# Kernel optimization log

Hardware: AMD Instinct MI355X
Metric: run time of the kernel (lower is better)

## Reference

```python
import jax, jax.numpy as jnp
import numpy as np

B = 32768
N_KPS = 14
DIM = N_KPS * 3   # 42
H1 = 1024
N_DOF = 7

# Fixed kinematic-chain constants (stand-in for the robot's link geometry,
# Franka-like link lengths; constants on device in the original).
LINK_LEN = jnp.array([0.333, 0.316, 0.384, 0.088, 0.107, 0.103, 0.100], dtype=jnp.float32)
OFF = jnp.array([0.05, 0.0, 0.0], dtype=jnp.float32)  # per-link auxiliary keypoint offset


def _rot_z(t):
    c, s = jnp.cos(t), jnp.sin(t)
    z, o = jnp.zeros_like(t), jnp.ones_like(t)
    return jnp.stack([jnp.stack([c, -s, z], -1),
                      jnp.stack([s, c, z], -1),
                      jnp.stack([z, z, o], -1)], -2)


def _rot_y(t):
    c, s = jnp.cos(t), jnp.sin(t)
    z, o = jnp.zeros_like(t), jnp.ones_like(t)
    return jnp.stack([jnp.stack([c, z, s], -1),
                      jnp.stack([z, o, z], -1),
                      jnp.stack([-s, z, c], -1)], -2)


def compute_3n_loss_42_rob(angles):
    """Forward kinematics: angles [B,7] -> keypoints [B,14,3].
    Alternating z/y revolute joints; 2 keypoints per link (origin + offset)."""
    Bn = angles.shape[0]
    R = jnp.broadcast_to(jnp.eye(3, dtype=angles.dtype), (Bn, 3, 3))
    p = jnp.zeros((Bn, 3), dtype=angles.dtype)
    pts = []
    for j in range(N_DOF):
        Rj = _rot_z(angles[:, j]) if j % 2 == 0 else _rot_y(angles[:, j])
        R = jnp.einsum('bij,bjk->bik', R, Rj)
        p = p + R @ jnp.array([0.0, 0.0, 1.0], dtype=angles.dtype) * LINK_LEN[j]
        pts.append(p)
        pts.append(p + R @ OFF)
    return jnp.stack(pts, axis=1)  # [B, 14, 3]


def compute_rede_rt(P, Q):
    """Batched Kabsch: rigid (R, t) minimizing ||R P + t - Q||. P,Q: [B,N,3]."""
    cp = P.mean(axis=1, keepdims=True)
    cq = Q.mean(axis=1, keepdims=True)
    H = jnp.einsum('bni,bnj->bij', P - cp, Q - cq)  # [B,3,3]
    U, S, Vt = jnp.linalg.svd(H)
    V = jnp.swapaxes(Vt, -1, -2)
    d = jnp.sign(jnp.linalg.det(jnp.einsum('bij,bkj->bik', V, U)))
    D = jnp.concatenate([jnp.ones((P.shape[0], 2), P.dtype), d[:, None]], axis=1)
    R = jnp.einsum('bij,bj,bkj->bik', V, D, U)  # V diag(1,1,d) U^T
    t = cq[:, 0] - jnp.einsum('bij,bj->bi', R, cp[:, 0])
    return R, t


def setup_inputs() -> dict:
    key = jax.random.key(0)
    k1, k2, k3, k4, k5 = jax.random.split(key, 5)
    return {
        'joints_3d_pred': jax.random.normal(k1, (B, N_KPS, 3), dtype=jnp.float32),
        'W1': jax.random.normal(k2, (DIM, H1), dtype=jnp.float32) * 0.05,
        'b1': jax.random.normal(k3, (H1,), dtype=jnp.float32) * 0.01,
        'W2': jax.random.normal(k4, (H1, N_DOF), dtype=jnp.float32) * 0.05,
        'b2': jax.random.normal(k5, (N_DOF,), dtype=jnp.float32) * 0.01,
    }


def reference(joints_3d_pred, W1, b1, W2, b2):
    # normalize to root keypoint
    norm = joints_3d_pred - joints_3d_pred[:, :1, :]          # [B,14,3]
    x = norm.reshape(norm.shape[0], -1)                        # [B,42]
    h = jax.nn.relu(x @ W1 + b1)                               # [B,1024]
    angles = h @ W2 + b2                                       # [B,7]
    all_dof_pred = angles[:, :, None]                          # [B,7,1]
    rob = compute_3n_loss_42_rob(angles)                       # [B,14,3]
    R, t = compute_rede_rt(rob, norm)
    t = t + joints_3d_pred[:, 0]                               # un-normalize translation
    top = jnp.concatenate([R, t[:, :, None]], axis=2)          # [B,3,4]
    bottom = jnp.broadcast_to(jnp.array([0.0, 0.0, 0.0, 1.0], dtype=R.dtype), (R.shape[0], 1, 4))
    pose = jnp.concatenate([top, bottom], axis=1)              # [B,4,4]
    return all_dof_pred, pose
```

## Files before the change

### kernel.cpp

```cpp
#include <hip/hip_runtime.h>
#include <math.h>

typedef __attribute__((ext_vector_type(8))) short short8;
typedef __attribute__((ext_vector_type(4))) float f32x4;
typedef __attribute__((ext_vector_type(2))) float f32x2;

constexpr int B_   = 32768;
constexpr int NKPS = 14;
constexpr int DIM  = 42;
constexpr int H1_  = 1024;
constexpr int NDOF = 7;

__device__ __forceinline__ unsigned short f2bf(float f) {
    unsigned u = __float_as_uint(f);
    u += 0x7FFFu + ((u >> 16) & 1u);
    return (unsigned short)(u >> 16);
}
__device__ __forceinline__ float bf2f(unsigned short h) {
    return __uint_as_float(((unsigned)h) << 16);
}

__global__ __launch_bounds__(256)
void prep_kernel(const float* __restrict__ W1, const float* __restrict__ b1,
                 const float* __restrict__ W2,
                 unsigned short* __restrict__ B1, float* __restrict__ W2p)
{
    const int T = blockIdx.x * 256 + threadIdx.x;
    if (T < 16384) {
        const int lane  = T & 63;
        const int ntile = (T >> 6) & 63;
        const int ks    = T >> 12;
        const int n     = ntile * 16 + (lane & 15);
        const int kbase = ks * 32 + ((lane >> 4) << 3);
        short8 s;
#pragma unroll
        for (int j = 0; j < 8; ++j) {
            const int k = kbase + j;
            unsigned short r;
            if (k < 42) {
                r = f2bf(W1[k * H1_ + n]);
            } else if (k < 84) {
                r = f2bf(W1[(k - 42) * H1_ + n]);
            } else if (k < 126) {
                const float x = W1[(k - 84) * H1_ + n];
                const unsigned short hi = f2bf(x);
                r = f2bf(x - bf2f(hi));
            } else if (k == 126) {
                r = f2bf(b1[n]);
            } else {
                const float x = b1[n];
                const unsigned short hi = f2bf(x);
                r = f2bf(x - bf2f(hi));
            }
            s[j] = (short)r;
        }
        *((short8*)(B1 + (long)T * 8)) = s;
    } else if (T < 16384 + 1024) {
        const int n = T - 16384;
#pragma unroll
        for (int d = 0; d < 7; ++d) W2p[n * 8 + d] = W2[n * 7 + d];
        W2p[n * 8 + 7] = 0.f;
    }
}

__global__ __launch_bounds__(512, 4)
void mlp_kernel(const float* __restrict__ joints,
                const unsigned short* __restrict__ B1,
                const float* __restrict__ W2p,
                const float* __restrict__ b2,
                float* __restrict__ outAng)
{
    __shared__ unsigned short Alds[32][136];
    __shared__ float sbuf[32][8];

    const int  tid = threadIdx.x;
    const long bm  = (long)blockIdx.x * 32;

    if (tid < 256) ((float*)sbuf)[tid] = 0.f;

    {
        const int r   = tid >> 4;
        const int c16 = tid & 15;
        const float* jr = joints + (bm + r) * DIM;
        short8 s;
#pragma unroll
        for (int j = 0; j < 8; ++j) {
            const int k = c16 * 8 + j;
            unsigned short v;
            if (k >= 126) {
                v = 0x3F80;
            } else {
                const int ksrc = (k < 42) ? k : (k < 84 ? k - 42 : k - 84);
                const float x = jr[ksrc] - jr[ksrc % 3];
                const unsigned short hi = f2bf(x);
                v = (k >= 42 && k < 84) ? f2bf(x - bf2f(hi)) : hi;
            }
            s[j] = (short)v;
        }
        *((short8*)&Alds[r][c16 * 8]) = s;
    }
    __syncthreads();

    const int lane = tid & 63;
    const int w    = tid >> 6;
    const int g    = lane >> 4;
    const int lm   = lane & 15;

    short8 a[2][4];
#pragma unroll
    for (int mt = 0; mt < 2; ++mt)
#pragma unroll
        for (int ks = 0; ks < 4; ++ks)
            a[mt][ks] = *((const short8*)&Alds[mt * 16 + lm][ks * 32 + g * 8]);

    f32x2 angp[2][4];
#pragma unroll
    for (int mt = 0; mt < 2; ++mt)
#pragma unroll
        for (int p = 0; p < 4; ++p) angp[mt][p] = (f32x2){0.f, 0.f};

    const short8* Bf = (const short8*)B1;
#pragma unroll
    for (int nt = 0; nt < 8; ++nt) {
        const int ntile = w * 8 + nt;
        f32x4 acc0 = (f32x4){0.f, 0.f, 0.f, 0.f};
        f32x4 acc1 = (f32x4){0.f, 0.f, 0.f, 0.f};
#pragma unroll
        for (int ks = 0; ks < 4; ++ks) {
            const short8 bfr = Bf[(ks * 64 + ntile) * 64 + lane];
            acc0 = __builtin_amdgcn_mfma_f32_16x16x32_bf16(bfr, a[0][ks], acc0, 0, 0, 0);
            acc1 = __builtin_amdgcn_mfma_f32_16x16x32_bf16(bfr, a[1][ks], acc1, 0, 0, 0);
        }
#pragma unroll
        for (int r = 0; r < 4; ++r) {
            const long n = (long)ntile * 16 + g * 4 + r;
            const f32x4 wa = *((const f32x4*)(W2p + n * 8));
            const f32x4 wb = *((const f32x4*)(W2p + n * 8 + 4));
            const f32x2 w01 = (f32x2){wa[0], wa[1]};
            const f32x2 w23 = (f32x2){wa[2], wa[3]};
            const f32x2 w45 = (f32x2){wb[0], wb[1]};
            const f32x2 w67 = (f32x2){wb[2], wb[3]};
            const float h0 = fmaxf(acc0[r], 0.f);
            const float h1 = fmaxf(acc1[r], 0.f);
            const f32x2 h0v = (f32x2){h0, h0};
            const f32x2 h1v = (f32x2){h1, h1};
            angp[0][0] = __builtin_elementwise_fma(h0v, w01, angp[0][0]);
            angp[0][1] = __builtin_elementwise_fma(h0v, w23, angp[0][1]);
            angp[0][2] = __builtin_elementwise_fma(h0v, w45, angp[0][2]);
            angp[0][3] = __builtin_elementwise_fma(h0v, w67, angp[0][3]);
            angp[1][0] = __builtin_elementwise_fma(h1v, w01, angp[1][0]);
            angp[1][1] = __builtin_elementwise_fma(h1v, w23, angp[1][1]);
            angp[1][2] = __builtin_elementwise_fma(h1v, w45, angp[1][2]);
            angp[1][3] = __builtin_elementwise_fma(h1v, w67, angp[1][3]);
        }
    }

    float red[2][8];
#pragma unroll
    for (int mt = 0; mt < 2; ++mt)
#pragma unroll
        for (int p = 0; p < 4; ++p) {
            red[mt][p * 2 + 0] = angp[mt][p][0];
            red[mt][p * 2 + 1] = angp[mt][p][1];
        }
#pragma unroll
    for (int mt = 0; mt < 2; ++mt)
#pragma unroll
        for (int i = 0; i < 8; ++i) {
            float v = red[mt][i];
            v += __shfl_xor(v, 16, 64);
            v += __shfl_xor(v, 32, 64);
            red[mt][i] = v;
        }
    if (lane < 16) {
#pragma unroll
        for (int mt = 0; mt < 2; ++mt)
#pragma unroll
            for (int i = 0; i < 8; ++i)
                atomicAdd(&sbuf[mt * 16 + lane][i], red[mt][i]);
    }
    __syncthreads();

    if (tid < 256) {
        const int m = tid >> 3, d = tid & 7;
        if (d < 7)
            outAng[(bm + m) * 7 + d] = sbuf[m][d] + b2[d];
    }
}

#define JROT(app, aqq, apq, arp, arq, v0p, v0q, v1p, v1q, v2p, v2q) do { \
    double _apq = (apq); \
    if (fabs(_apq) > 1e-300) { \
        double _tau = ((aqq) - (app)) / (2.0 * _apq); \
        double _t = ((_tau >= 0.0) ? 1.0 : -1.0) / (fabs(_tau) + sqrt(1.0 + _tau*_tau)); \
        double _c = 1.0 / sqrt(1.0 + _t*_t); \
        double _s = _t * _c; \
        (app) -= _t * _apq; \
        (aqq) += _t * _apq; \
        (apq) = 0.0; \
        { double _rp = (arp), _rq = (arq); \
          (arp) = _c*_rp - _s*_rq; (arq) = _s*_rp + _c*_rq; } \
        { double _v = (v0p); (v0p) = _c*_v - _s*(v0q); (v0q) = _s*_v + _c*(v0q); } \
        { double _v = (v1p); (v1p) = _c*_v - _s*(v1q); (v1q) = _s*_v + _c*(v1q); } \
        { double _v = (v2p); (v2p) = _c*_v - _s*(v2q); (v2q) = _s*_v + _c*(v2q); } \
    } \
} while (0)

#define SWAP_EIG(ea, eb, va0, vb0, va1, vb1, va2, vb2) do { \
    double _tm; \
    _tm = (ea); (ea) = (eb); (eb) = _tm; \
    _tm = (va0); (va0) = (vb0); (vb0) = _tm; \
    _tm = (va1); (va1) = (vb1); (vb1) = _tm; \
    _tm = (va2); (va2) = (vb2); (vb2) = _tm; \
} while (0)

__global__ __launch_bounds__(256)
void fk_kernel(const float* __restrict__ joints,
               const float* __restrict__ ang_in,
               float* __restrict__ out)
{
    const int b = blockIdx.x * 256 + threadIdx.x;
    if (b >= B_) return;

    const float* jr = joints + (long)b * DIM;
    const float j0x = jr[0], j0y = jr[1], j0z = jr[2];
    float q[DIM];
#pragma unroll
    for (int k = 0; k < NKPS; ++k) {
        q[3*k+0] = jr[3*k+0] - j0x;
        q[3*k+1] = jr[3*k+1] - j0y;
        q[3*k+2] = jr[3*k+2] - j0z;
    }

    float ang[NDOF];
#pragma unroll
    for (int d = 0; d < NDOF; ++d) ang[d] = ang_in[(long)b * NDOF + d];

    float R00=1.f,R01=0.f,R02=0.f, R10=0.f,R11=1.f,R12=0.f, R20=0.f,R21=0.f,R22=1.f;
    float px=0.f, py=0.f, pz=0.f;
    float Hr00=0.f,Hr01=0.f,Hr02=0.f,Hr10=0.f,Hr11=0.f,Hr12=0.f,Hr20=0.f,Hr21=0.f,Hr22=0.f;
    float sPx=0.f, sPy=0.f, sPz=0.f;
    const float LL[NDOF] = {0.333f,0.316f,0.384f,0.088f,0.107f,0.103f,0.1f};

#pragma unroll
    for (int j = 0; j < NDOF; ++j) {
        float s, c;
        sincosf(ang[j], &s, &c);
        if ((j & 1) == 0) {
            float a0=R00, a1=R01; R00 = c*a0 + s*a1; R01 = c*a1 - s*a0;
            float b0=R10, b1v=R11; R10 = c*b0 + s*b1v; R11 = c*b1v - s*b0;
            float c0=R20, c1=R21; R20 = c*c0 + s*c1; R21 = c*c1 - s*c0;
        } else {
            float a0=R00, a2=R02; R00 = c*a0 - s*a2; R02 = s*a0 + c*a2;
            float b0=R10, b2v=R12; R10 = c*b0 - s*b2v; R12 = s*b0 + c*b2v;
            float c0=R20, c2=R22; R20 = c*c0 - s*c2; R22 = s*c0 + c*c2;
        }
        px = fmaf(LL[j], R02, px);
        py = fmaf(LL[j], R12, py);
        pz = fmaf(LL[j], R22, pz);
        {
            const float qx = q[6*j+0], qy = q[6*j+1], qz = q[6*j+2];
            sPx += px; sPy += py; sPz += pz;
            Hr00 = fmaf(px, qx, Hr00); Hr01 = fmaf(px, qy, Hr01); Hr02 = fmaf(px, qz, Hr02);
            Hr10 = fmaf(py, qx, Hr10); Hr11 = fmaf(py, qy, Hr11); Hr12 = fmaf(py, qz, Hr12);
            Hr20 = fmaf(pz, qx, Hr20); Hr21 = fmaf(pz, qy, Hr21); Hr22 = fmaf(pz, qz, Hr22);
        }
        {
            const float ox = fmaf(0.05f, R00, px);
            const float oy = fmaf(0.05f, R10, py);
            const float oz = fmaf(0.05f, R20, pz);
            const float qx = q[6*j+3], qy = q[6*j+4], qz = q[6*j+5];
            sPx += ox; sPy += oy; sPz += oz;
            Hr00 = fmaf(ox, qx, Hr00); Hr01 = fmaf(ox, qy, Hr01); Hr02 = fmaf(ox, qz, Hr02);
            Hr10 = fmaf(oy, qx, Hr10); Hr11 = fmaf(oy, qy, Hr11); Hr12 = fmaf(oy, qz, Hr12);
            Hr20 = fmaf(oz, qx, Hr20); Hr21 = fmaf(oz, qy, Hr21); Hr22 = fmaf(oz, qz, Hr22);
        }
    }

    float sQx = 0.f, sQy = 0.f, sQz = 0.f;
#pragma unroll
    for (int n = 0; n < NKPS; ++n) { sQx += q[3*n+0]; sQy += q[3*n+1]; sQz += q[3*n+2]; }

    const double inv14 = 1.0 / 14.0;
    const double cpx = (double)sPx * inv14, cpy = (double)sPy * inv14, cpz = (double)sPz * inv14;
    const double cqx = (double)sQx * inv14, cqy = (double)sQy * inv14, cqz = (double)sQz * inv14;

    const double h00 = (double)Hr00 - 14.0*cpx*cqx, h01 = (double)Hr01 - 14.0*cpx*cqy, h02 = (double)Hr02 - 14.0*cpx*cqz;
    const double h10 = (double)Hr10 - 14.0*cpy*cqx, h11 = (double)Hr11 - 14.0*cpy*cqy, h12 = (double)Hr12 - 14.0*cpy*cqz;
    const double h20 = (double)Hr20 - 14.0*cpz*cqx, h21 = (double)Hr21 - 14.0*cpz*cqy, h22 = (double)Hr22 - 14.0*cpz*cqz;

    double m00 = h00*h00 + h10*h10 + h20*h20;
    double m01 = h00*h01 + h10*h11 + h20*h21;
    double m02 = h00*h02 + h10*h12 + h20*h22;
    double m11 = h01*h01 + h11*h11 + h21*h21;
    double m12 = h01*h02 + h11*h12 + h21*h22;
    double m22 = h02*h02 + h12*h12 + h22*h22;

    double v00=1.0, v01=0.0, v02=0.0;
    double v10=0.0, v11=1.0, v12=0.0;
    double v20=0.0, v21=0.0, v22=1.0;

#pragma unroll
    for (int sw = 0; sw < 5; ++sw) {
        JROT(m00, m11, m01, m02, m12, v00, v01, v10, v11, v20, v21);
        JROT(m00, m22, m02, m01, m12, v00, v02, v10, v12, v20, v22);
        JROT(m11, m22, m12, m01, m02, v01, v02, v11, v12, v21, v22);
    }

    double e0 = m00, e1 = m11, e2 = m22;
    if (e0 < e1) SWAP_EIG(e0, e1, v00, v01, v10, v11, v20, v21);
    if (e0 < e2) SWAP_EIG(e0, e2, v00, v02, v10, v12, v20, v22);
    if (e1 < e2) SWAP_EIG(e1, e2, v01, v02, v11, v12, v21, v22);

    const double s0 = sqrt(fmax(e0, 0.0));
    const double s1 = sqrt(fmax(e1, 0.0));
    const double s2 = sqrt(fmax(e2, 0.0));

    const double det = h00*(h11*h22 - h12*h21) - h01*(h10*h22 - h12*h20) + h02*(h10*h21 - h11*h20);
    const double dsg = (det >= 0.0) ? 1.0 : -1.0;

    const double tiny = 1e-30;
    const double g0 = 1.0 / fmax(s0, tiny);
    const double g1 = 1.0 / fmax(s1, tiny);
    const double g2 = dsg / fmax(s2, tiny);

    const double K00 = g0*v00*v00 + g1*v01*v01 + g2*v02*v02;
    const double K01 = g0*v00*v10 + g1*v01*v11 + g2*v02*v12;
    const double K02 = g0*v00*v20 + g1*v01*v21 + g2*v02*v22;
    const double K11 = g0*v10*v10 + g1*v11*v11 + g2*v12*v12;
    const double K12 = g0*v10*v20 + g1*v11*v21 + g2*v12*v22;
    const double K22 = g0*v20*v20 + g1*v21*v21 + g2*v22*v22;

    const double r00 = K00*h00 + K01*h01 + K02*h02;
    const double r01 = K00*h10 + K01*h11 + K02*h12;
    const double r02 = K00*h20 + K01*h21 + K02*h22;
    const double r10 = K01*h00 + K11*h01 + K12*h02;
    const double r11 = K01*h10 + K11*h11 + K12*h12;
    const double r12 = K01*h20 + K11*h21 + K12*h22;
    const double r20 = K02*h00 + K12*h01 + K22*h02;
    const double r21 = K02*h10 + K12*h11 + K22*h12;
    const double r22 = K02*h20 + K12*h21 + K22*h22;

    const double tx = cqx - (r00*cpx + r01*cpy + r02*cpz) + (double)j0x;
    const double ty = cqy - (r10*cpx + r11*cpy + r12*cpz) + (double)j0y;
    const double tz = cqz - (r20*cpx + r21*cpy + r22*cpz) + (double)j0z;

    float* po = out + (long)B_ * NDOF + (long)b * 16;
    po[0]  = (float)r00; po[1]  = (float)r01; po[2]  = (float)r02; po[3]  = (float)tx;
    po[4]  = (float)r10; po[5]  = (float)r11; po[6]  = (float)r12; po[7]  = (float)ty;
    po[8]  = (float)r20; po[9]  = (float)r21; po[10] = (float)r22; po[11] = (float)tz;
    po[12] = 0.f; po[13] = 0.f; po[14] = 0.f; po[15] = 1.f;
}

extern "C" void kernel_launch(void* const* d_in, const int* in_sizes, int n_in,
                              void* d_out, int out_size, void* d_ws, size_t ws_size,
                              hipStream_t stream) {
    const float* joints = (const float*)d_in[0];
    const float* W1     = (const float*)d_in[1];
    const float* b1     = (const float*)d_in[2];
    const float* W2     = (const float*)d_in[3];
    const float* b2     = (const float*)d_in[4];
    float* out = (float*)d_out;

    unsigned short* B1  = (unsigned short*)d_ws;
    float*          W2p = (float*)((char*)d_ws + 262144);

    hipLaunchKernelGGL(prep_kernel, dim3(68), dim3(256), 0, stream,
                       W1, b1, W2, B1, W2p);

    hipLaunchKernelGGL(mlp_kernel, dim3(B_ / 32), dim3(512), 0, stream,
                       joints, B1, W2p, b2, out);

    hipLaunchKernelGGL(fk_kernel, dim3(B_ / 256), dim3(256), 0, stream,
                       joints, out, out);
}
```

Baseline: 50.54 us.

## Prefetch next B1 tile into registers and stage W2 in swizzled LDS

The change issues the W1 (B1) fragment loads for the first n-tile before the input-staging phase, then double-buffers them so the next tile's loads are in flight while the current tile's MFMAs run. It also copies the padded W2 (32 KB) into shared memory with an XOR swizzle, so the second layer reads from LDS rather than global memory. The aim is to hide global load latency and cut repeated global W2 traffic. The cost is 32 KB more LDS per block, which with 512 threads and a target of 4 blocks per CU may lower occupancy, plus extra registers for the prefetch buffers.

Result: faster. 48.78 us (-3.5%).

```diff
diff --git a/kernel.cpp b/kernel.cpp
--- a/kernel.cpp
+++ b/kernel.cpp
@@ -72,9 +72,28 @@
 {
     __shared__ unsigned short Alds[32][136];
     __shared__ float sbuf[32][8];
-
-    const int  tid = threadIdx.x;
-    const long bm  = (long)blockIdx.x * 32;
+    __shared__ float W2s[8192];
+
+    const int  tid  = threadIdx.x;
+    const long bm   = (long)blockIdx.x * 32;
+    const int  lane = tid & 63;
+    const int  w    = tid >> 6;
+    const int  g    = lane >> 4;
+    const int  lm   = lane & 15;
+
+    const short8* Bf = (const short8*)B1;
+    short8 bc[4];
+#pragma unroll
+    for (int ks = 0; ks < 4; ++ks)
+        bc[ks] = Bf[(ks * 64 + w * 8) * 64 + lane];
+
+#pragma unroll
+    for (int i = 0; i < 4; ++i) {
+        const int a  = (i * 512 + tid) * 16;
+        const f32x4 v = *((const f32x4*)((const char*)W2p + a));
+        const int sw = a ^ (((a >> 7) & 3) << 4);
+        *((f32x4*)((char*)W2s + sw)) = v;
+    }
 
     if (tid < 256) ((float*)sbuf)[tid] = 0.f;
 
@@ -101,11 +120,6 @@
     }
     __syncthreads();
 
-    const int lane = tid & 63;
-    const int w    = tid >> 6;
-    const int g    = lane >> 4;
-    const int lm   = lane & 15;
-
     short8 a[2][4];
 #pragma unroll
     for (int mt = 0; mt < 2; ++mt)
@@ -119,23 +133,31 @@
 #pragma unroll
         for (int p = 0; p < 4; ++p) angp[mt][p] = (f32x2){0.f, 0.f};
 
-    const short8* Bf = (const short8*)B1;
 #pragma unroll
     for (int nt = 0; nt < 8; ++nt) {
-        const int ntile = w * 8 + nt;
+        short8 bn[4];
+        if (nt < 7) {
+#pragma unroll
+            for (int ks = 0; ks < 4; ++ks)
+                bn[ks] = Bf[(ks * 64 + w * 8 + nt + 1) * 64 + lane];
+        }
+
         f32x4 acc0 = (f32x4){0.f, 0.f, 0.f, 0.f};
         f32x4 acc1 = (f32x4){0.f, 0.f, 0.f, 0.f};
 #pragma unroll
         for (int ks = 0; ks < 4; ++ks) {
-            const short8 bfr = Bf[(ks * 64 + ntile) * 64 + lane];
-            acc0 = __builtin_amdgcn_mfma_f32_16x16x32_bf16(bfr, a[0][ks], acc0, 0, 0, 0);
-            acc1 = __builtin_amdgcn_mfma_f32_16x16x32_bf16(bfr, a[1][ks], acc1, 0, 0, 0);
-        }
+            acc0 = __builtin_amdgcn_mfma_f32_16x16x32_bf16(bc[ks], a[0][ks], acc0, 0, 0, 0);
+            acc1 = __builtin_amdgcn_mfma_f32_16x16x32_bf16(bc[ks], a[1][ks], acc1, 0, 0, 0);
+        }
+
+        const int ntile = w * 8 + nt;
 #pragma unroll
         for (int r = 0; r < 4; ++r) {
-            const long n = (long)ntile * 16 + g * 4 + r;
-            const f32x4 wa = *((const f32x4*)(W2p + n * 8));
-            const f32x4 wb = *((const f32x4*)(W2p + n * 8 + 4));
+            const int n  = ntile * 16 + g * 4 + r;
+            const int ad = n * 32;
+            const int sw = ad ^ (((ad >> 7) & 3) << 4);
+            const f32x4 wa = *((const f32x4*)((const char*)W2s + sw));
+            const f32x4 wb = *((const f32x4*)((const char*)W2s + (sw ^ 16)));
             const f32x2 w01 = (f32x2){wa[0], wa[1]};
             const f32x2 w23 = (f32x2){wa[2], wa[3]};
             const f32x2 w45 = (f32x2){wb[0], wb[1]};
@@ -152,6 +174,11 @@
             angp[1][1] = __builtin_elementwise_fma(h1v, w23, angp[1][1]);
             angp[1][2] = __builtin_elementwise_fma(h1v, w45, angp[1][2]);
             angp[1][3] = __builtin_elementwise_fma(h1v, w67, angp[1][3]);
+        }
+
+        if (nt < 7) {
+#pragma unroll
+            for (int ks = 0; ks < 4; ++ks) bc[ks] = bn[ks];
         }
     }
 
```

## Fuse MLP and FK/Kabsch kernels, switch to fp16 MFMA, halve waves per block

Applied to the files above, without the earlier changes.

Merges the MLP and forward-kinematics/Kabsch kernels into one kernel. After the MLP reduction, 32 threads per block read the angles straight from shared memory and compute the pose, which removes a launch and the round trip of the angles through global memory. Changes the split-precision operands from bf16 to fp16 and uses the f16 MFMA. Cuts the block from 512 to 256 threads, so each wave covers 16 N-tiles and loads its B fragments ahead of the MFMAs. The risk is that the serial double-precision Kabsch step, now run by only 32 threads per block, sits on the critical path of the MLP blocks and lowers utilisation.

New measurement: 55.73 us. 10.3% more time.

```diff
diff --git a/kernel.cpp b/kernel.cpp
--- a/kernel.cpp
+++ b/kernel.cpp
@@ -1,7 +1,7 @@
 #include <hip/hip_runtime.h>
 #include <math.h>
 
-typedef __attribute__((ext_vector_type(8))) short short8;
+typedef __attribute__((ext_vector_type(8))) _Float16 half8;
 typedef __attribute__((ext_vector_type(4))) float f32x4;
 typedef __attribute__((ext_vector_type(2))) float f32x2;
 
@@ -11,19 +11,10 @@
 constexpr int H1_  = 1024;
 constexpr int NDOF = 7;
 
-__device__ __forceinline__ unsigned short f2bf(float f) {
-    unsigned u = __float_as_uint(f);
-    u += 0x7FFFu + ((u >> 16) & 1u);
-    return (unsigned short)(u >> 16);
-}
-__device__ __forceinline__ float bf2f(unsigned short h) {
-    return __uint_as_float(((unsigned)h) << 16);
-}
-
 __global__ __launch_bounds__(256)
 void prep_kernel(const float* __restrict__ W1, const float* __restrict__ b1,
                  const float* __restrict__ W2,
-                 unsigned short* __restrict__ B1, float* __restrict__ W2p)
+                 _Float16* __restrict__ B1f, float* __restrict__ W2p)
 {
     const int T = blockIdx.x * 256 + threadIdx.x;
     if (T < 16384) {
@@ -32,29 +23,29 @@
         const int ks    = T >> 12;
         const int n     = ntile * 16 + (lane & 15);
         const int kbase = ks * 32 + ((lane >> 4) << 3);
-        short8 s;
+        half8 s;
 #pragma unroll
         for (int j = 0; j < 8; ++j) {
             const int k = kbase + j;
-            unsigned short r;
+            _Float16 hv;
             if (k < 42) {
-                r = f2bf(W1[k * H1_ + n]);
+                hv = (_Float16)W1[k * H1_ + n];
             } else if (k < 84) {
-                r = f2bf(W1[(k - 42) * H1_ + n]);
+                hv = (_Float16)W1[(k - 42) * H1_ + n];
             } else if (k < 126) {
                 const float x = W1[(k - 84) * H1_ + n];
-                const unsigned short hi = f2bf(x);
-                r = f2bf(x - bf2f(hi));
+                const _Float16 hi = (_Float16)x;
+                hv = (_Float16)(x - (float)hi);
             } else if (k == 126) {
-                r = f2bf(b1[n]);
+                hv = (_Float16)b1[n];
             } else {
                 const float x = b1[n];
-                const unsigned short hi = f2bf(x);
-                r = f2bf(x - bf2f(hi));
-            }
-            s[j] = (short)r;
-        }
-        *((short8*)(B1 + (long)T * 8)) = s;
+                const _Float16 hi = (_Float16)x;
+                hv = (_Float16)(x - (float)hi);
+            }
+            s[j] = hv;
+        }
+        *((half8*)(B1f + (long)T * 8)) = s;
     } else if (T < 16384 + 1024) {
         const int n = T - 16384;
 #pragma unroll
@@ -63,55 +54,89 @@
     }
 }
 
-__global__ __launch_bounds__(512, 4)
-void mlp_kernel(const float* __restrict__ joints,
-                const unsigned short* __restrict__ B1,
-                const float* __restrict__ W2p,
-                const float* __restrict__ b2,
-                float* __restrict__ outAng)
+#define JROT(app, aqq, apq, arp, arq, v0p, v0q, v1p, v1q, v2p, v2q) do { \
+    double _apq = (apq); \
+    if (fabs(_apq) > 1e-300) { \
+        double _tau = ((aqq) - (app)) / (2.0 * _apq); \
+        double _t = ((_tau >= 0.0) ? 1.0 : -1.0) / (fabs(_tau) + sqrt(1.0 + _tau*_tau)); \
+        double _c = 1.0 / sqrt(1.0 + _t*_t); \
+        double _s = _t * _c; \
+        (app) -= _t * _apq; \
+        (aqq) += _t * _apq; \
+        (apq) = 0.0; \
+        { double _rp = (arp), _rq = (arq); \
+          (arp) = _c*_rp - _s*_rq; (arq) = _s*_rp + _c*_rq; } \
+        { double _v = (v0p); (v0p) = _c*_v - _s*(v0q); (v0q) = _s*_v + _c*(v0q); } \
+        { double _v = (v1p); (v1p) = _c*_v - _s*(v1q); (v1q) = _s*_v + _c*(v1q); } \
+        { double _v = (v2p); (v2p) = _c*_v - _s*(v2q); (v2q) = _s*_v + _c*(v2q); } \
+    } \
+} while (0)
+
+#define SWAP_EIG(ea, eb, va0, vb0, va1, vb1, va2, vb2) do { \
+    double _tm; \
+    _tm = (ea); (ea) = (eb); (eb) = _tm; \
+    _tm = (va0); (va0) = (vb0); (vb0) = _tm; \
+    _tm = (va1); (va1) = (vb1); (vb1) = _tm; \
+    _tm = (va2); (va2) = (vb2); (vb2) = _tm; \
+} while (0)
+
+__global__ __launch_bounds__(256, 4)
+void mlp_fk_kernel(const float* __restrict__ joints,
+                   const _Float16* __restrict__ B1f,
+                   const float* __restrict__ W2p,
+                   const float* __restrict__ b2,
+                   float* __restrict__ out)
 {
-    __shared__ unsigned short Alds[32][136];
+    __shared__ _Float16 Alds[32][136];
     __shared__ float sbuf[32][8];
 
-    const int  tid = threadIdx.x;
-    const long bm  = (long)blockIdx.x * 32;
-
-    if (tid < 256) ((float*)sbuf)[tid] = 0.f;
+    const int  tid  = threadIdx.x;
+    const long bm   = (long)blockIdx.x * 32;
+    const int  lane = tid & 63;
+    const int  w    = tid >> 6;
+    const int  g    = lane >> 4;
+    const int  lm   = lane & 15;
+
+    ((float*)sbuf)[tid] = 0.f;
 
     {
-        const int r   = tid >> 4;
-        const int c16 = tid & 15;
+        const int r  = tid >> 3;
+        const int c8 = tid & 7;
         const float* jr = joints + (bm + r) * DIM;
-        short8 s;
-#pragma unroll
-        for (int j = 0; j < 8; ++j) {
-            const int k = c16 * 8 + j;
-            unsigned short v;
-            if (k >= 126) {
-                v = 0x3F80;
-            } else {
-                const int ksrc = (k < 42) ? k : (k < 84 ? k - 42 : k - 84);
-                const float x = jr[ksrc] - jr[ksrc % 3];
-                const unsigned short hi = f2bf(x);
-                v = (k >= 42 && k < 84) ? f2bf(x - bf2f(hi)) : hi;
-            }
-            s[j] = (short)v;
-        }
-        *((short8*)&Alds[r][c16 * 8]) = s;
+#pragma unroll
+        for (int h2 = 0; h2 < 2; ++h2) {
+            const int gi = c8 + h2 * 8;
+            half8 s;
+#pragma unroll
+            for (int j = 0; j < 8; ++j) {
+                const int k = gi * 8 + j;
+                _Float16 hv;
+                if (k < 42) {
+                    hv = (_Float16)(jr[k] - jr[k % 3]);
+                } else if (k < 84) {
+                    const int km = k - 42;
+                    const float x = jr[km] - jr[km % 3];
+                    const _Float16 hi = (_Float16)x;
+                    hv = (_Float16)(x - (float)hi);
+                } else if (k < 126) {
+                    const int km = k - 84;
+                    hv = (_Float16)(jr[km] - jr[km % 3]);
+                } else {
+                    hv = (_Float16)1.0f;
+                }
+                s[j] = hv;
+            }
+            *((half8*)&Alds[r][gi * 8]) = s;
+        }
     }
     __syncthreads();
 
-    const int lane = tid & 63;
-    const int w    = tid >> 6;
-    const int g    = lane >> 4;
-    const int lm   = lane & 15;
-
-    short8 a[2][4];
+    half8 a[2][4];
 #pragma unroll
     for (int mt = 0; mt < 2; ++mt)
 #pragma unroll
         for (int ks = 0; ks < 4; ++ks)
-            a[mt][ks] = *((const short8*)&Alds[mt * 16 + lm][ks * 32 + g * 8]);
+            a[mt][ks] = *((const half8*)&Alds[mt * 16 + lm][ks * 32 + g * 8]);
 
     f32x2 angp[2][4];
 #pragma unroll
@@ -119,18 +144,23 @@
 #pragma unroll
         for (int p = 0; p < 4; ++p) angp[mt][p] = (f32x2){0.f, 0.f};
 
-    const short8* Bf = (const short8*)B1;
-#pragma unroll
-    for (int nt = 0; nt < 8; ++nt) {
-        const int ntile = w * 8 + nt;
+    const half8* Bf = (const half8*)B1f;
+#pragma unroll 4
+    for (int nt = 0; nt < 16; ++nt) {
+        const int ntile = w * 16 + nt;
+        half8 bc[4];
+#pragma unroll
+        for (int ks = 0; ks < 4; ++ks)
+            bc[ks] = Bf[(ks * 64 + ntile) * 64 + lane];
+
         f32x4 acc0 = (f32x4){0.f, 0.f, 0.f, 0.f};
         f32x4 acc1 = (f32x4){0.f, 0.f, 0.f, 0.f};
 #pragma unroll
         for (int ks = 0; ks < 4; ++ks) {
-            const short8 bfr = Bf[(ks * 64 + ntile) * 64 + lane];
-            acc0 = __builtin_amdgcn_mfma_f32_16x16x32_bf16(bfr, a[0][ks], acc0, 0, 0, 0);
-            acc1 = __builtin_amdgcn_mfma_f32_16x16x32_bf16(bfr, a[1][ks], acc1, 0, 0, 0);
-        }
+            acc0 = __builtin_amdgcn_mfma_f32_16x16x32_f16(bc[ks], a[0][ks], acc0, 0, 0, 0);
+            acc1 = __builtin_amdgcn_mfma_f32_16x16x32_f16(bc[ks], a[1][ks], acc1, 0, 0, 0);
+        }
+
 #pragma unroll
         for (int r = 0; r < 4; ++r) {
             const long n = (long)ntile * 16 + g * 4 + r;
@@ -181,175 +211,135 @@
     }
     __syncthreads();
 
-    if (tid < 256) {
+    {
         const int m = tid >> 3, d = tid & 7;
         if (d < 7)
-            outAng[(bm + m) * 7 + d] = sbuf[m][d] + b2[d];
-    }
-}
-
-#define JROT(app, aqq, apq, arp, arq, v0p, v0q, v1p, v1q, v2p, v2q) do { \
-    double _apq = (apq); \
-    if (fabs(_apq) > 1e-300) { \
-        double _tau = ((aqq) - (app)) / (2.0 * _apq); \
-        double _t = ((_tau >= 0.0) ? 1.0 : -1.0) / (fabs(_tau) + sqrt(1.0 + _tau*_tau)); \
-        double _c = 1.0 / sqrt(1.0 + _t*_t); \
-        double _s = _t * _c; \
-        (app) -= _t * _apq; \
-        (aqq) += _t * _apq; \
-        (apq) = 0.0; \
-        { double _rp = (arp), _rq = (arq); \
-          (arp) = _c*_rp - _s*_rq; (arq) = _s*_rp + _c*_rq; } \
-        { double _v = (v0p); (v0p) = _c*_v - _s*(v0q); (v0q) = _s*_v + _c*(v0q); } \
-        { double _v = (v1p); (v1p) = _c*_v - _s*(v1q); (v1q) = _s*_v + _c*(v1q); } \
-        { double _v = (v2p); (v2p) = _c*_v - _s*(v2q); (v2q) = _s*_v + _c*(v2q); } \
-    } \
-} while (0)
-
-#define SWAP_EIG(ea, eb, va0, vb0, va1, vb1, va2, vb2) do { \
-    double _tm; \
-    _tm = (ea); (ea) = (eb); (eb) = _tm; \
-    _tm = (va0); (va0) = (vb0); (vb0) = _tm; \
-    _tm = (va1); (va1) = (vb1); (vb1) = _tm; \
-    _tm = (va2); (va2) = (vb2); (vb2) = _tm; \
-} while (0)
-
-__global__ __launch_bounds__(256)
-void fk_kernel(const float* __restrict__ joints,
-               const float* __restrict__ ang_in,
-               float* __restrict__ out)
-{
-    const int b = blockIdx.x * 256 + threadIdx.x;
-    if (b >= B_) return;
-
-    const float* jr = joints + (long)b * DIM;
-    const float j0x = jr[0], j0y = jr[1], j0z = jr[2];
-    float q[DIM];
-#pragma unroll
-    for (int k = 0; k < NKPS; ++k) {
-        q[3*k+0] = jr[3*k+0] - j0x;
-        q[3*k+1] = jr[3*k+1] - j0y;
-        q[3*k+2] = jr[3*k+2] - j0z;
-    }
-
-    float ang[NDOF];
-#pragma unroll
-    for (int d = 0; d < NDOF; ++d) ang[d] = ang_in[(long)b * NDOF + d];
-
-    float R00=1.f,R01=0.f,R02=0.f, R10=0.f,R11=1.f,R12=0.f, R20=0.f,R21=0.f,R22=1.f;
-    float px=0.f, py=0.f, pz=0.f;
-    float Hr00=0.f,Hr01=0.f,Hr02=0.f,Hr10=0.f,Hr11=0.f,Hr12=0.f,Hr20=0.f,Hr21=0.f,Hr22=0.f;
-    float sPx=0.f, sPy=0.f, sPz=0.f;
-    const float LL[NDOF] = {0.333f,0.316f,0.384f,0.088f,0.107f,0.103f,0.1f};
-
-#pragma unroll
-    for (int j = 0; j < NDOF; ++j) {
-        float s, c;
-        sincosf(ang[j], &s, &c);
-        if ((j & 1) == 0) {
-            float a0=R00, a1=R01; R00 = c*a0 + s*a1; R01 = c*a1 - s*a0;
-            float b0=R10, b1v=R11; R10 = c*b0 + s*b1v; R11 = c*b1v - s*b0;
-            float c0=R20, c1=R21; R20 = c*c0 + s*c1; R21 = c*c1 - s*c0;
-        } else {
-            float a0=R00, a2=R02; R00 = c*a0 - s*a2; R02 = s*a0 + c*a2;
-            float b0=R10, b2v=R12; R10 = c*b0 - s*b2v; R12 = s*b0 + c*b2v;
-            float c0=R20, c2=R22; R20 = c*c0 - s*c2; R22 = s*c0 + c*c2;
-        }
-        px = fmaf(LL[j], R02, px);
-        py = fmaf(LL[j], R12, py);
-        pz = fmaf(LL[j], R22, pz);
-        {
-            const float qx = q[6*j+0], qy = q[6*j+1], qz = q[6*j+2];
-            sPx += px; sPy += py; sPz += pz;
-            Hr00 = fmaf(px, qx, Hr00); Hr01 = fmaf(px, qy, Hr01); Hr02 = fmaf(px, qz, Hr02);
-            Hr10 = fmaf(py, qx, Hr10); Hr11 = fmaf(py, qy, Hr11); Hr12 = fmaf(py, qz, Hr12);
-            Hr20 = fmaf(pz, qx, Hr20); Hr21 = fmaf(pz, qy, Hr21); Hr22 = fmaf(pz, qz, Hr22);
-        }
-        {
-            const float ox = fmaf(0.05f, R00, px);
-            const float oy = fmaf(0.05f, R10, py);
-            const float oz = fmaf(0.05f, R20, pz);
-            const float qx = q[6*j+3], qy = q[6*j+4], qz = q[6*j+5];
-            sPx += ox; sPy += oy; sPz += oz;
-            Hr00 = fmaf(ox, qx, Hr00); Hr01 = fmaf(ox, qy, Hr01); Hr02 = fmaf(ox, qz, Hr02);
-            Hr10 = fmaf(oy, qx, Hr10); Hr11 = fmaf(oy, qy, Hr11); Hr12 = fmaf(oy, qz, Hr12);
-            Hr20 = fmaf(oz, qx, Hr20); Hr21 = fmaf(oz, qy, Hr21); Hr22 = fmaf(oz, qz, Hr22);
-        }
-    }
-
-    float sQx = 0.f, sQy = 0.f, sQz = 0.f;
-#pragma unroll
-    for (int n = 0; n < NKPS; ++n) { sQx += q[3*n+0]; sQy += q[3*n+1]; sQz += q[3*n+2]; }
-
-    const double inv14 = 1.0 / 14.0;
-    const double cpx = (double)sPx * inv14, cpy = (double)sPy * inv14, cpz = (double)sPz * inv14;
-    const double cqx = (double)sQx * inv14, cqy = (double)sQy * inv14, cqz = (double)sQz * inv14;
-
-    const double h00 = (double)Hr00 - 14.0*cpx*cqx, h01 = (double)Hr01 - 14.0*cpx*cqy, h02 = (double)Hr02 - 14.0*cpx*cqz;
-    const double h10 = (double)Hr10 - 14.0*cpy*cqx, h11 = (double)Hr11 - 14.0*cpy*cqy, h12 = (double)Hr12 - 14.0*cpy*cqz;
-    const double h20 = (double)Hr20 - 14.0*cpz*cqx, h21 = (double)Hr21 - 14.0*cpz*cqy, h22 = (double)Hr22 - 14.0*cpz*cqz;
-
-    double m00 = h00*h00 + h10*h10 + h20*h20;
-    double m01 = h00*h01 + h10*h11 + h20*h21;
-    double m02 = h00*h02 + h10*h12 + h20*h22;
-    double m11 = h01*h01 + h11*h11 + h21*h21;
-    double m12 = h01*h02 + h11*h12 + h21*h22;
-    double m22 = h02*h02 + h12*h12 + h22*h22;
-
-    double v00=1.0, v01=0.0, v02=0.0;
-    double v10=0.0, v11=1.0, v12=0.0;
-    double v20=0.0, v21=0.0, v22=1.0;
-
-#pragma unroll
-    for (int sw = 0; sw < 5; ++sw) {
-        JROT(m00, m11, m01, m02, m12, v00, v01, v10, v11, v20, v21);
-        JROT(m00, m22, m02, m01, m12, v00, v02, v10, v12, v20, v22);
-        JROT(m11, m22, m12, m01, m02, v01, v02, v11, v12, v21, v22);
-    }
-
-    double e0 = m00, e1 = m11, e2 = m22;
-    if (e0 < e1) SWAP_EIG(e0, e1, v00, v01, v10, v11, v20, v21);
-    if (e0 < e2) SWAP_EIG(e0, e2, v00, v02, v10, v12, v20, v22);
-    if (e1 < e2) SWAP_EIG(e1, e2, v01, v02, v11, v12, v21, v22);
-
-    const double s0 = sqrt(fmax(e0, 0.0));
-    const double s1 = sqrt(fmax(e1, 0.0));
-    const double s2 = sqrt(fmax(e2, 0.0));
-
-    const double det = h00*(h11*h22 - h12*h21) - h01*(h10*h22 - h12*h20) + h02*(h10*h21 - h11*h20);
-    const double dsg = (det >= 0.0) ? 1.0 : -1.0;
-
-    const double tiny = 1e-30;
-    const double g0 = 1.0 / fmax(s0, tiny);
-    const double g1 = 1.0 / fmax(s1, tiny);
-    const double g2 = dsg / fmax(s2, tiny);
-
-    const double K00 = g0*v00*v00 + g1*v01*v01 + g2*v02*v02;
-    const double K01 = g0*v00*v10 + g1*v01*v11 + g2*v02*v12;
-    const double K02 = g0*v00*v20 + g1*v01*v21 + g2*v02*v22;
-    const double K11 = g0*v10*v10 + g1*v11*v11 + g2*v12*v12;
-    const double K12 = g0*v10*v20 + g1*v11*v21 + g2*v12*v22;
-    const double K22 = g0*v20*v20 + g1*v21*v21 + g2*v22*v22;
-
-    const double r00 = K00*h00 + K01*h01 + K02*h02;
-    const double r01 = K00*h10 + K01*h11 + K02*h12;
-    const double r02 = K00*h20 + K01*h21 + K02*h22;
-    const double r10 = K01*h00 + K11*h01 + K12*h02;
-    const double r11 = K01*h10 + K11*h11 + K12*h12;
-    const double r12 = K01*h20 + K11*h21 + K12*h22;
-    const double r20 = K02*h00 + K12*h01 + K22*h02;
-    const double r21 = K02*h10 + K12*h11 + K22*h12;
-    const double r22 = K02*h20 + K12*h21 + K22*h22;
-
-    const double tx = cqx - (r00*cpx + r01*cpy + r02*cpz) + (double)j0x;
-    const double ty = cqy - (r10*cpx + r11*cpy + r12*cpz) + (double)j0y;
-    const double tz = cqz - (r20*cpx + r21*cpy + r22*cpz) + (double)j0z;
-
-    float* po = out + (long)B_ * NDOF + (long)b * 16;
-    po[0]  = (float)r00; po[1]  = (float)r01; po[2]  = (float)r02; po[3]  = (float)tx;
-    po[4]  = (float)r10; po[5]  = (float)r11; po[6]  = (float)r12; po[7]  = (float)ty;
-    po[8]  = (float)r20; po[9]  = (float)r21; po[10] = (float)r22; po[11] = (float)tz;
-    po[12] = 0.f; po[13] = 0.f; po[14] = 0.f; po[15] = 1.f;
+            out[(bm + m) * 7 + d] = sbuf[m][d] + b2[d];
+    }
+
+    if (tid < 32) {
+        const long b = bm + tid;
+        const float* jr = joints + b * DIM;
+        const float j0x = jr[0], j0y = jr[1], j0z = jr[2];
+
+        float ang[NDOF];
+#pragma unroll
+        for (int d = 0; d < NDOF; ++d) ang[d] = sbuf[tid][d] + b2[d];
+
+        float R00=1.f,R01=0.f,R02=0.f, R10=0.f,R11=1.f,R12=0.f, R20=0.f,R21=0.f,R22=1.f;
+        float px=0.f, py=0.f, pz=0.f;
+        float Hr00=0.f,Hr01=0.f,Hr02=0.f,Hr10=0.f,Hr11=0.f,Hr12=0.f,Hr20=0.f,Hr21=0.f,Hr22=0.f;
+        float sPx=0.f, sPy=0.f, sPz=0.f;
+        float sQx=0.f, sQy=0.f, sQz=0.f;
+        const float LL[NDOF] = {0.333f,0.316f,0.384f,0.088f,0.107f,0.103f,0.1f};
+
+#pragma unroll
+        for (int j = 0; j < NDOF; ++j) {
+            float s, c;
+            sincosf(ang[j], &s, &c);
+            if ((j & 1) == 0) {
+                float a0=R00, a1=R01; R00 = c*a0 + s*a1; R01 = c*a1 - s*a0;
+                float b0=R10, b1v=R11; R10 = c*b0 + s*b1v; R11 = c*b1v - s*b0;
+                float c0=R20, c1=R21; R20 = c*c0 + s*c1; R21 = c*c1 - s*c0;
+            } else {
+                float a0=R00, a2=R02; R00 = c*a0 - s*a2; R02 = s*a0 + c*a2;
+                float b0=R10, b2v=R12; R10 = c*b0 - s*b2v; R12 = s*b0 + c*b2v;
+                float c0=R20, c2=R22; R20 = c*c0 - s*c2; R22 = s*c0 + c*c2;
+            }
+            px = fmaf(LL[j], R02, px);
+            py = fmaf(LL[j], R12, py);
+            pz = fmaf(LL[j], R22, pz);
+            {
+                const float qx = jr[6*j+0] - j0x, qy = jr[6*j+1] - j0y, qz = jr[6*j+2] - j0z;
+                sQx += qx; sQy += qy; sQz += qz;
+                sPx += px; sPy += py; sPz += pz;
+                Hr00 = fmaf(px, qx, Hr00); Hr01 = fmaf(px, qy, Hr01); Hr02 = fmaf(px, qz, Hr02);
+                Hr10 = fmaf(py, qx, Hr10); Hr11 = fmaf(py, qy, Hr11); Hr12 = fmaf(py, qz, Hr12);
+                Hr20 = fmaf(pz, qx, Hr20); Hr21 = fmaf(pz, qy, Hr21); Hr22 = fmaf(pz, qz, Hr22);
+            }
+            {
+                const float ox = fmaf(0.05f, R00, px);
+                const float oy = fmaf(0.05f, R10, py);
+                const float oz = fmaf(0.05f, R20, pz);
+                const float qx = jr[6*j+3] - j0x, qy = jr[6*j+4] - j0y, qz = jr[6*j+5] - j0z;
+                sQx += qx; sQy += qy; sQz += qz;
+                sPx += ox; sPy += oy; sPz += oz;
+                Hr00 = fmaf(ox, qx, Hr00); Hr01 = fmaf(ox, qy, Hr01); Hr02 = fmaf(ox, qz, Hr02);
+                Hr10 = fmaf(oy, qx, Hr10); Hr11 = fmaf(oy, qy, Hr11); Hr12 = fmaf(oy, qz, Hr12);
+                Hr20 = fmaf(oz, qx, Hr20); Hr21 = fmaf(oz, qy, Hr21); Hr22 = fmaf(oz, qz, Hr22);
+            }
+        }
+
+        const double inv14 = 1.0 / 14.0;
+        const double cpx = (double)sPx * inv14, cpy = (double)sPy * inv14, cpz = (double)sPz * inv14;
+        const double cqx = (double)sQx * inv14, cqy = (double)sQy * inv14, cqz = (double)sQz * inv14;
+
+        const double h00 = (double)Hr00 - 14.0*cpx*cqx, h01 = (double)Hr01 - 14.0*cpx*cqy, h02 = (double)Hr02 - 14.0*cpx*cqz;
+        const double h10 = (double)Hr10 - 14.0*cpy*cqx, h11 = (double)Hr11 - 14.0*cpy*cqy, h12 = (double)Hr12 - 14.0*cpy*cqz;
+        const double h20 = (double)Hr20 - 14.0*cpz*cqx, h21 = (double)Hr21 - 14.0*cpz*cqy, h22 = (double)Hr22 - 14.0*cpz*cqz;
+
+        double m00 = h00*h00 + h10*h10 + h20*h20;
+        double m01 = h00*h01 + h10*h11 + h20*h21;
+        double m02 = h00*h02 + h10*h12 + h20*h22;
+        double m11 = h01*h01 + h11*h11 + h21*h21;
+        double m12 = h01*h02 + h11*h12 + h21*h22;
+        double m22 = h02*h02 + h12*h12 + h22*h22;
+
+        double v00=1.0, v01=0.0, v02=0.0;
+        double v10=0.0, v11=1.0, v12=0.0;
+        double v20=0.0, v21=0.0, v22=1.0;
+
+#pragma unroll
+        for (int sw = 0; sw < 5; ++sw) {
+            JROT(m00, m11, m01, m02, m12, v00, v01, v10, v11, v20, v21);
+            JROT(m00, m22, m02, m01, m12, v00, v02, v10, v12, v20, v22);
+            JROT(m11, m22, m12, m01, m02, v01, v02, v11, v12, v21, v22);
+        }
+
+        double e0 = m00, e1 = m11, e2 = m22;
+        if (e0 < e1) SWAP_EIG(e0, e1, v00, v01, v10, v11, v20, v21);
+        if (e0 < e2) SWAP_EIG(e0, e2, v00, v02, v10, v12, v20, v22);
+        if (e1 < e2) SWAP_EIG(e1, e2, v01, v02, v11, v12, v21, v22);
+
+        const double s0 = sqrt(fmax(e0, 0.0));
+        const double s1 = sqrt(fmax(e1, 0.0));
+        const double s2 = sqrt(fmax(e2, 0.0));
+
+        const double det = h00*(h11*h22 - h12*h21) - h01*(h10*h22 - h12*h20) + h02*(h10*h21 - h11*h20);
+        const double dsg = (det >= 0.0) ? 1.0 : -1.0;
+
+        const double tiny = 1e-30;
+        const double g0 = 1.0 / fmax(s0, tiny);
+        const double g1 = 1.0 / fmax(s1, tiny);
+        const double g2 = dsg / fmax(s2, tiny);
+
+        const double K00 = g0*v00*v00 + g1*v01*v01 + g2*v02*v02;
+        const double K01 = g0*v00*v10 + g1*v01*v11 + g2*v02*v12;
+        const double K02 = g0*v00*v20 + g1*v01*v21 + g2*v02*v22;
+        const double K11 = g0*v10*v10 + g1*v11*v11 + g2*v12*v12;
+        const double K12 = g0*v10*v20 + g1*v11*v21 + g2*v12*v22;
+        const double K22 = g0*v20*v20 + g1*v21*v21 + g2*v22*v22;
+
+        const double r00 = K00*h00 + K01*h01 + K02*h02;
+        const double r01 = K00*h10 + K01*h11 + K02*h12;
+        const double r02 = K00*h20 + K01*h21 + K02*h22;
+        const double r10 = K01*h00 + K11*h01 + K12*h02;
+        const double r11 = K01*h10 + K11*h11 + K12*h12;
+        const double r12 = K01*h20 + K11*h21 + K12*h22;
+        const double r20 = K02*h00 + K12*h01 + K22*h02;
+        const double r21 = K02*h10 + K12*h11 + K22*h12;
+        const double r22 = K02*h20 + K12*h21 + K22*h22;
+
+        const double tx = cqx - (r00*cpx + r01*cpy + r02*cpz) + (double)j0x;
+        const double ty = cqy - (r10*cpx + r11*cpy + r12*cpz) + (double)j0y;
+        const double tz = cqz - (r20*cpx + r21*cpy + r22*cpz) + (double)j0z;
+
+        float* po = out + (long)B_ * NDOF + b * 16;
+        po[0]  = (float)r00; po[1]  = (float)r01; po[2]  = (float)r02; po[3]  = (float)tx;
+        po[4]  = (float)r10; po[5]  = (float)r11; po[6]  = (float)r12; po[7]  = (float)ty;
+        po[8]  = (float)r20; po[9]  = (float)r21; po[10] = (float)r22; po[11] = (float)tz;
+        po[12] = 0.f; po[13] = 0.f; po[14] = 0.f; po[15] = 1.f;
+    }
 }
 
 extern "C" void kernel_launch(void* const* d_in, const int* in_sizes, int n_in,
@@ -362,15 +352,12 @@
     const float* b2     = (const float*)d_in[4];
     float* out = (float*)d_out;
 
-    unsigned short* B1  = (unsigned short*)d_ws;
-    float*          W2p = (float*)((char*)d_ws + 262144);
+    _Float16* B1f = (_Float16*)d_ws;
+    float*    W2p = (float*)((char*)d_ws + 262144);
 
     hipLaunchKernelGGL(prep_kernel, dim3(68), dim3(256), 0, stream,
-                       W1, b1, W2, B1, W2p);
-
-    hipLaunchKernelGGL(mlp_kernel, dim3(B_ / 32), dim3(512), 0, stream,
-                       joints, B1, W2p, b2, out);
-
-    hipLaunchKernelGGL(fk_kernel, dim3(B_ / 256), dim3(256), 0, stream,
-                       joints, out, out);
+                       W1, b1, W2, B1f, W2p);
+
+    hipLaunchKernelGGL(mlp_fk_kernel, dim3(B_ / 32), dim3(256), 0, stream,
+                       joints, B1f, W2p, b2, out);
 }
```
